# Kernel tuning notes

Hardware: AMD Instinct MI355X
Metric: run time of the kernel (lower is better)

The kernel has to match this reference:

```python
import jax, jax.numpy as jnp
import numpy as np

GRID_SIZE = 5
SPLINE_ORDER = 3
NUM_BASIS = GRID_SIZE + SPLINE_ORDER  # 8
GRID = jnp.linspace(-1.0, 1.0, GRID_SIZE + 2 * SPLINE_ORDER + 1)  # [12]
EPS = 1e-6


def bspline_basis(x):
    """Iterative Cox-de Boor. x: [...]; returns [..., NUM_BASIS]."""
    xe = x[..., None]
    # order-0 indicator basis: [..., G-1]
    B = ((xe >= GRID[:-1]) & (xe < GRID[1:])).astype(x.dtype)
    for k in range(1, SPLINE_ORDER + 1):
        nb = B.shape[-1] - 1
        g_i = GRID[:nb]
        g_i1 = GRID[1:1 + nb]
        g_ik = GRID[k:k + nb]
        g_ik1 = GRID[k + 1:k + 1 + nb]
        dl = g_ik - g_i
        dr = g_ik1 - g_i1
        left = jnp.where(dl > EPS, (xe - g_i) / jnp.where(dl > EPS, dl, 1.0), 0.0) * B[..., :nb]
        right = jnp.where(dr > EPS, (g_ik1 - xe) / jnp.where(dr > EPS, dr, 1.0), 0.0) * B[..., 1:nb + 1]
        B = left + right
    return B[..., :NUM_BASIS]


def setup_inputs() -> dict:
    key = jax.random.key(0)
    k1, k2 = jax.random.split(key)
    x = jax.random.normal(k1, (8192, 512), dtype=jnp.float32)
    spline_coeffs = jax.random.normal(k2, (512, 512, NUM_BASIS), dtype=jnp.float32) * 0.1
    return {"x": x, "spline_coeffs": spline_coeffs}


def reference(x, spline_coeffs):
    xn = jnp.tanh(x)                       # [B, in]
    basis = bspline_basis(xn)              # [B, in, K]
    # output[b, o] = sum_{i,k} coeffs[o, i, k] * basis[b, i, k]
    return jnp.einsum('bik,oik->bo', basis, spline_coeffs)
```

## Files before the change

kernel.cpp:

```cpp
#include <hip/hip_runtime.h>
#include <hip/hip_bf16.h>
#include <stdint.h>


#define M_TOTAL 8192
#define N_DIM   512
#define K_DIM   4096
#define BM 128
#define BN 128
#define BK 64
#define NT_HALF 32
#define GRP_LDS 65536
#define BUF_HALF 32768

typedef __attribute__((ext_vector_type(8))) short short8;
typedef __attribute__((ext_vector_type(4))) float f32x4;

typedef const __attribute__((address_space(1))) uint32_t ga_u32;
typedef __attribute__((address_space(3))) uint32_t ls_u32;

__device__ __forceinline__ void gload_lds16(const void* g, void* l) {
  __builtin_amdgcn_global_load_lds((ga_u32*)(uintptr_t)g,
                                   (ls_u32*)(uint32_t)(uintptr_t)l, 16, 0, 0);
}

__device__ __forceinline__ uint32_t f2bf(float f) {
  uint32_t u = __builtin_bit_cast(uint32_t, f);
  return (u + 0x7FFFu + ((u >> 16) & 1u)) >> 16;
}

__device__ __forceinline__ void basis_slots(float xv, uint32_t o[4]) {
  xv = fminf(15.f, fmaxf(-15.f, xv));
  float e  = __expf(2.0f * xv);
  float t  = (e - 1.0f) * __builtin_amdgcn_rcpf(e + 1.0f);
  float uf = (t + 1.0f) * 5.5f;
  int   c  = (int)uf;  c = c > 10 ? 10 : c;
  float u  = uf - (float)c;
  float u2 = u * u, u3 = u2 * u, om = 1.0f - u;
  float w0 = om * om * om * (1.0f / 6.0f);
  float w1 = (3.0f * u3 - 6.0f * u2 + 4.0f) * (1.0f / 6.0f);
  float w2 = (-3.0f * u3 + 3.0f * u2 + 3.0f * u + 1.0f) * (1.0f / 6.0f);
  float w3 = u3 * (1.0f / 6.0f);
  uint32_t p01 = f2bf(w0) | (f2bf(w1) << 16);
  uint32_t p23 = f2bf(w2) | (f2bf(w3) << 16);
  uint64_t W = (uint64_t)p01 | ((uint64_t)p23 << 32);
  int d = c - 3;
  uint64_t lo = (d < 0) ? (W >> ((-d) * 16))
              : ((d < 4) ? (W << (d * 16)) : 0ull);
  uint64_t hi = (d <= 0) ? 0ull
              : ((d < 4) ? (W >> ((4 - d) * 16)) : (W << ((d - 4) * 16)));
  o[0] = (uint32_t)lo; o[1] = (uint32_t)(lo >> 32);
  o[2] = (uint32_t)hi; o[3] = (uint32_t)(hi >> 32);
}

__global__ __launch_bounds__(256) void cvt_kernel(const float* __restrict__ c,
                                                  __hip_bfloat16* __restrict__ Bt,
                                                  int total8) {
  int idx = blockIdx.x * 256 + threadIdx.x;
  if (idx >= total8) return;
  const float4* cp = reinterpret_cast<const float4*>(c) + (size_t)idx * 2;
  float4 a = cp[0], b = cp[1];
  union { unsigned short us[8]; int4 v; } pk;
  pk.us[0] = f2bf(a.x); pk.us[1] = f2bf(a.y);
  pk.us[2] = f2bf(a.z); pk.us[3] = f2bf(a.w);
  pk.us[4] = f2bf(b.x); pk.us[5] = f2bf(b.y);
  pk.us[6] = f2bf(b.z); pk.us[7] = f2bf(b.w);
  reinterpret_cast<int4*>(Bt)[idx] = pk.v;
}

__global__ __launch_bounds__(512, 2) void fused_kernel(
    const float* __restrict__ x,
    const __hip_bfloat16* __restrict__ Bt,
    float* __restrict__ C) {
  __shared__ char lds[2 * GRP_LDS];

  const int tid   = threadIdx.x;
  const int wid   = tid >> 6;
  const int lane  = tid & 63;
  const int quad  = lane >> 4;
  const int l16   = lane & 15;
  const int kgrp  = wid >> 2;
  const int w2    = wid & 3;
  const int waveM = w2 >> 1, waveN = w2 & 1;
  const int tg    = tid & 255;

  int b = blockIdx.x;
  int mt = (b & 7) * 8 + ((b >> 3) >> 2);
  int nt = (b >> 3) & 3;
  const int m0 = mt * BM, n0 = nt * BN;

  char* grp = lds + kgrp * GRP_LDS;

  uint32_t bGlob[4], sOff[4], xBase[4], aWr[4];
#pragma unroll
  for (int t = 0; t < 4; ++t) {
    int s = t * 256 + tg, row = s >> 3, p = s & 7;
    sOff[t]  = (uint32_t)s * 16u;
    bGlob[t] = (uint32_t)(n0 + row) * K_DIM + (uint32_t)(p ^ (row & 7)) * 8u
             + (uint32_t)kgrp * 2048u;
    xBase[t] = (uint32_t)(m0 + row) * 512u + (uint32_t)kgrp * 256u + (uint32_t)p;
    aWr[t]   = (uint32_t)(row * 8 + (p ^ (row & 7))) * 16u;
  }

  uint32_t aOff[2][4], bOff[2][4];
#pragma unroll
  for (int kk = 0; kk < 2; ++kk) {
    int c = kk * 4 + quad;
#pragma unroll
    for (int mi = 0; mi < 4; ++mi) {
      int row = waveM * 64 + mi * 16 + l16;
      aOff[kk][mi] = (uint32_t)(row * 8 + (c ^ (row & 7))) * 16u;
    }
#pragma unroll
    for (int ni = 0; ni < 4; ++ni) {
      int row = waveN * 64 + ni * 16 + l16;
      bOff[kk][ni] = 16384u + (uint32_t)(row * 8 + (c ^ (row & 7))) * 16u;
    }
  }

  f32x4 acc[4][4];
#pragma unroll
  for (int mi = 0; mi < 4; ++mi)
#pragma unroll
    for (int ni = 0; ni < 4; ++ni)
      acc[mi][ni] = (f32x4){0.f, 0.f, 0.f, 0.f};

#pragma unroll
  for (int t = 0; t < 4; ++t)
    gload_lds16(Bt + bGlob[t], grp + 16384 + sOff[t]);
#pragma unroll
  for (int t = 0; t < 4; ++t) {
    uint32_t o[4]; basis_slots(x[xBase[t]], o);
    *reinterpret_cast<int4*>(grp + aWr[t]) = make_int4(o[0], o[1], o[2], o[3]);
  }

  for (int it = 0; it < NT_HALF; ++it) {
    const int cur = it & 1;
    char* bufc = grp + cur * BUF_HALF;
    __syncthreads();
    if (it + 1 < NT_HALF) {
      char* bufn = grp + (1 - cur) * BUF_HALF;
      uint32_t kOff = (uint32_t)(it + 1) * 64u;
#pragma unroll
      for (int t = 0; t < 4; ++t)
        gload_lds16(Bt + bGlob[t] + kOff, bufn + 16384 + sOff[t]);
#pragma unroll
      for (int t = 0; t < 4; ++t) {
        uint32_t o[4]; basis_slots(x[xBase[t] + (uint32_t)(it + 1) * 8u], o);
        *reinterpret_cast<int4*>(bufn + aWr[t]) = make_int4(o[0], o[1], o[2], o[3]);
      }
    }
#pragma unroll
    for (int kk = 0; kk < 2; ++kk) {
      short8 af[4], bf[4];
#pragma unroll
      for (int mi = 0; mi < 4; ++mi)
        af[mi] = *reinterpret_cast<const short8*>(bufc + aOff[kk][mi]);
#pragma unroll
      for (int ni = 0; ni < 4; ++ni)
        bf[ni] = *reinterpret_cast<const short8*>(bufc + bOff[kk][ni]);
#pragma unroll
      for (int mi = 0; mi < 4; ++mi)
#pragma unroll
        for (int ni = 0; ni < 4; ++ni)
          acc[mi][ni] = __builtin_amdgcn_mfma_f32_16x16x32_bf16(
              af[mi], bf[ni], acc[mi][ni], 0, 0, 0);
    }
  }

  __syncthreads();
  if (kgrp == 1) {
#pragma unroll
    for (int mi = 0; mi < 4; ++mi)
#pragma unroll
      for (int ni = 0; ni < 4; ++ni) {
        int f = mi * 4 + ni;
        *reinterpret_cast<f32x4*>(lds + w2 * 16384 + f * 1024 + lane * 16) =
            acc[mi][ni];
      }
  }
  __syncthreads();
  if (kgrp == 0) {
#pragma unroll
    for (int mi = 0; mi < 4; ++mi) {
#pragma unroll
      for (int ni = 0; ni < 4; ++ni) {
        int f = mi * 4 + ni;
        f32x4 other = *reinterpret_cast<f32x4*>(
            lds + w2 * 16384 + f * 1024 + lane * 16);
        f32x4 s = acc[mi][ni] + other;
        int col = n0 + waveN * 64 + ni * 16 + l16;
#pragma unroll
        for (int r = 0; r < 4; ++r) {
          int row = m0 + waveM * 64 + mi * 16 + quad * 4 + r;
          C[(size_t)row * N_DIM + col] = s[r];
        }
      }
    }
  }
}

extern "C" void kernel_launch(void* const* d_in, const int* in_sizes, int n_in,
                              void* d_out, int out_size, void* d_ws, size_t ws_size,
                              hipStream_t stream) {
  const float* x    = (const float*)d_in[0];
  const float* coef = (const float*)d_in[1];
  float* out = (float*)d_out;

  __hip_bfloat16* Bt = (__hip_bfloat16*)d_ws;

  const int total8 = N_DIM * K_DIM / 8;
  cvt_kernel<<<(total8 + 255) / 256, 256, 0, stream>>>(coef, Bt, total8);

  fused_kernel<<<(M_TOTAL / BM) * (N_DIM / BN), 512, 0, stream>>>(x, Bt, out);
}
```

Before: 147.6 us.

## Split basis computation into separate kernel and use split-K GEMM with atomics

Replaces the fused kernel, which computed B-spline bases inline while loading the weights, with a standalone basis kernel that writes a bf16 A matrix to workspace. A 256-thread GEMM kernel then streams both A and B through LDS with async global-to-LDS loads, splitting K four ways and combining partial sums with float atomic adds into a pre-zeroed output. The M dimension is processed in two halves so the A workspace can be reused. This adds extra launches, a memset, a round trip of A through memory, and atomic traffic, in exchange for more blocks and a simpler GEMM inner loop.

```diff
diff --git a/kernel.cpp b/kernel.cpp
--- a/kernel.cpp
+++ b/kernel.cpp
@@ -9,9 +9,11 @@
 #define BM 128
 #define BN 128
 #define BK 64
-#define NT_HALF 32
-#define GRP_LDS 65536
-#define BUF_HALF 32768
+#define KSPLIT 4
+#define MHALF  4096
+#define KCHUNK (K_DIM / KSPLIT)
+#define NT     (KCHUNK / BK)
+#define BUF_BYTES ((BM + BN) * BK * 2)
 
 typedef __attribute__((ext_vector_type(8))) short short8;
 typedef __attribute__((ext_vector_type(4))) float f32x4;
@@ -53,6 +55,16 @@
   o[2] = (uint32_t)hi; o[3] = (uint32_t)(hi >> 32);
 }
 
+__global__ __launch_bounds__(256) void basis_kernel(const float* __restrict__ x,
+                                                    __hip_bfloat16* __restrict__ A,
+                                                    int total) {
+  int idx = blockIdx.x * 256 + threadIdx.x;
+  if (idx >= total) return;
+  uint32_t o[4];
+  basis_slots(x[idx], o);
+  reinterpret_cast<int4*>(A)[idx] = make_int4(o[0], o[1], o[2], o[3]);
+}
+
 __global__ __launch_bounds__(256) void cvt_kernel(const float* __restrict__ c,
                                                   __hip_bfloat16* __restrict__ Bt,
                                                   int total8) {
@@ -61,45 +73,44 @@
   const float4* cp = reinterpret_cast<const float4*>(c) + (size_t)idx * 2;
   float4 a = cp[0], b = cp[1];
   union { unsigned short us[8]; int4 v; } pk;
-  pk.us[0] = f2bf(a.x); pk.us[1] = f2bf(a.y);
-  pk.us[2] = f2bf(a.z); pk.us[3] = f2bf(a.w);
-  pk.us[4] = f2bf(b.x); pk.us[5] = f2bf(b.y);
-  pk.us[6] = f2bf(b.z); pk.us[7] = f2bf(b.w);
+  pk.us[0] = (unsigned short)f2bf(a.x); pk.us[1] = (unsigned short)f2bf(a.y);
+  pk.us[2] = (unsigned short)f2bf(a.z); pk.us[3] = (unsigned short)f2bf(a.w);
+  pk.us[4] = (unsigned short)f2bf(b.x); pk.us[5] = (unsigned short)f2bf(b.y);
+  pk.us[6] = (unsigned short)f2bf(b.z); pk.us[7] = (unsigned short)f2bf(b.w);
   reinterpret_cast<int4*>(Bt)[idx] = pk.v;
 }
 
-__global__ __launch_bounds__(512, 2) void fused_kernel(
-    const float* __restrict__ x,
+__global__ __launch_bounds__(256) void gemm_kernel(
+    const __hip_bfloat16* __restrict__ A,
     const __hip_bfloat16* __restrict__ Bt,
     float* __restrict__ C) {
-  __shared__ char lds[2 * GRP_LDS];
+  __shared__ __hip_bfloat16 lds[2 * (BM + BN) * BK];
 
   const int tid   = threadIdx.x;
   const int wid   = tid >> 6;
   const int lane  = tid & 63;
   const int quad  = lane >> 4;
   const int l16   = lane & 15;
-  const int kgrp  = wid >> 2;
-  const int w2    = wid & 3;
-  const int waveM = w2 >> 1, waveN = w2 & 1;
-  const int tg    = tid & 255;
-
-  int b = blockIdx.x;
-  int mt = (b & 7) * 8 + ((b >> 3) >> 2);
-  int nt = (b >> 3) & 3;
-  const int m0 = mt * BM, n0 = nt * BN;
-
-  char* grp = lds + kgrp * GRP_LDS;
-
-  uint32_t bGlob[4], sOff[4], xBase[4], aWr[4];
+  const int waveM = wid >> 1;
+  const int waveN = wid & 1;
+
+  const int b   = blockIdx.x;
+  const int xcd = b & 7;
+  const int q   = b >> 3;
+  const int mt  = xcd * 4 + (q >> 4);
+  const int nt  = (q >> 2) & 3;
+  const int ks  = q & 3;
+  const int m0  = mt * BM;
+  const int n0  = nt * BN;
+  const uint32_t kbase = (uint32_t)ks * KCHUNK;
+
+  uint32_t aGlob[4], bGlob[4], sOff[4];
 #pragma unroll
   for (int t = 0; t < 4; ++t) {
-    int s = t * 256 + tg, row = s >> 3, p = s & 7;
+    int s = t * 256 + tid, row = s >> 3, p = s & 7, cc = p ^ (row & 7);
     sOff[t]  = (uint32_t)s * 16u;
-    bGlob[t] = (uint32_t)(n0 + row) * K_DIM + (uint32_t)(p ^ (row & 7)) * 8u
-             + (uint32_t)kgrp * 2048u;
-    xBase[t] = (uint32_t)(m0 + row) * 512u + (uint32_t)kgrp * 256u + (uint32_t)p;
-    aWr[t]   = (uint32_t)(row * 8 + (p ^ (row & 7))) * 16u;
+    aGlob[t] = (uint32_t)(m0 + row) * K_DIM + (uint32_t)cc * 8u + kbase;
+    bGlob[t] = (uint32_t)(n0 + row) * K_DIM + (uint32_t)cc * 8u + kbase;
   }
 
   uint32_t aOff[2][4], bOff[2][4];
@@ -118,6 +129,8 @@
     }
   }
 
+  char* ldsc = (char*)lds;
+
   f32x4 acc[4][4];
 #pragma unroll
   for (int mi = 0; mi < 4; ++mi)
@@ -126,28 +139,22 @@
       acc[mi][ni] = (f32x4){0.f, 0.f, 0.f, 0.f};
 
 #pragma unroll
-  for (int t = 0; t < 4; ++t)
-    gload_lds16(Bt + bGlob[t], grp + 16384 + sOff[t]);
-#pragma unroll
   for (int t = 0; t < 4; ++t) {
-    uint32_t o[4]; basis_slots(x[xBase[t]], o);
-    *reinterpret_cast<int4*>(grp + aWr[t]) = make_int4(o[0], o[1], o[2], o[3]);
-  }
-
-  for (int it = 0; it < NT_HALF; ++it) {
+    gload_lds16(A + aGlob[t], ldsc + sOff[t]);
+    gload_lds16(Bt + bGlob[t], ldsc + 16384 + sOff[t]);
+  }
+
+  for (int it = 0; it < NT; ++it) {
     const int cur = it & 1;
-    char* bufc = grp + cur * BUF_HALF;
+    char* bufc = ldsc + cur * BUF_BYTES;
     __syncthreads();
-    if (it + 1 < NT_HALF) {
-      char* bufn = grp + (1 - cur) * BUF_HALF;
-      uint32_t kOff = (uint32_t)(it + 1) * 64u;
-#pragma unroll
-      for (int t = 0; t < 4; ++t)
-        gload_lds16(Bt + bGlob[t] + kOff, bufn + 16384 + sOff[t]);
+    if (it + 1 < NT) {
+      char* bufn = ldsc + (1 - cur) * BUF_BYTES;
+      uint32_t kt = (uint32_t)(it + 1) * BK;
 #pragma unroll
       for (int t = 0; t < 4; ++t) {
-        uint32_t o[4]; basis_slots(x[xBase[t] + (uint32_t)(it + 1) * 8u], o);
-        *reinterpret_cast<int4*>(bufn + aWr[t]) = make_int4(o[0], o[1], o[2], o[3]);
+        gload_lds16(A + aGlob[t] + kt, bufn + sOff[t]);
+        gload_lds16(Bt + bGlob[t] + kt, bufn + 16384 + sOff[t]);
       }
     }
 #pragma unroll
@@ -168,33 +175,15 @@
     }
   }
 
-  __syncthreads();
-  if (kgrp == 1) {
-#pragma unroll
-    for (int mi = 0; mi < 4; ++mi)
-#pragma unroll
-      for (int ni = 0; ni < 4; ++ni) {
-        int f = mi * 4 + ni;
-        *reinterpret_cast<f32x4*>(lds + w2 * 16384 + f * 1024 + lane * 16) =
-            acc[mi][ni];
-      }
-  }
-  __syncthreads();
-  if (kgrp == 0) {
-#pragma unroll
-    for (int mi = 0; mi < 4; ++mi) {
-#pragma unroll
-      for (int ni = 0; ni < 4; ++ni) {
-        int f = mi * 4 + ni;
-        f32x4 other = *reinterpret_cast<f32x4*>(
-            lds + w2 * 16384 + f * 1024 + lane * 16);
-        f32x4 s = acc[mi][ni] + other;
-        int col = n0 + waveN * 64 + ni * 16 + l16;
-#pragma unroll
-        for (int r = 0; r < 4; ++r) {
-          int row = m0 + waveM * 64 + mi * 16 + quad * 4 + r;
-          C[(size_t)row * N_DIM + col] = s[r];
-        }
+#pragma unroll
+  for (int mi = 0; mi < 4; ++mi) {
+#pragma unroll
+    for (int ni = 0; ni < 4; ++ni) {
+      int col = n0 + waveN * 64 + ni * 16 + l16;
+#pragma unroll
+      for (int r = 0; r < 4; ++r) {
+        int row = m0 + waveM * 64 + mi * 16 + quad * 4 + r;
+        unsafeAtomicAdd(&C[(size_t)row * N_DIM + col], acc[mi][ni][r]);
       }
     }
   }
@@ -208,9 +197,18 @@
   float* out = (float*)d_out;
 
   __hip_bfloat16* Bt = (__hip_bfloat16*)d_ws;
+  __hip_bfloat16* A  = (__hip_bfloat16*)((char*)d_ws + (size_t)4 * 1024 * 1024);
+
+  hipMemsetAsync(d_out, 0, (size_t)out_size * sizeof(float), stream);
 
   const int total8 = N_DIM * K_DIM / 8;
   cvt_kernel<<<(total8 + 255) / 256, 256, 0, stream>>>(coef, Bt, total8);
 
-  fused_kernel<<<(M_TOTAL / BM) * (N_DIM / BN), 512, 0, stream>>>(x, Bt, out);
-}
+  for (int half = 0; half < 2; ++half) {
+    const int total = MHALF * 512;
+    basis_kernel<<<total / 256, 256, 0, stream>>>(
+        x + (size_t)half * MHALF * 512, A, total);
+    gemm_kernel<<<(MHALF / BM) * (N_DIM / BN) * KSPLIT, 256, 0, stream>>>(
+        A, Bt, out + (size_t)half * MHALF * N_DIM);
+  }
+}
```

New measurement: 172.8 us. 17.0% more time.

## Unfuse B-spline basis computation into a separate kernel feeding a pure GEMM

Applied to the files above, without the earlier changes.

Moves the tanh and B-spline basis evaluation out of the GEMM mainloop into a standalone kernel that writes a bf16 A matrix (8192x4096) to workspace. The GEMM then loads both A and B tiles with async global-to-LDS loads instead of computing basis values in registers and storing them to LDS. This removes per-tile ALU work and the four-way recomputation of the basis across N tiles, at the cost of an extra kernel launch and writing then reading a 64 MB intermediate. The launch bounds also drop the min-2-blocks hint.

```diff
diff --git a/kernel.cpp b/kernel.cpp
--- a/kernel.cpp
+++ b/kernel.cpp
@@ -53,6 +53,16 @@
   o[2] = (uint32_t)hi; o[3] = (uint32_t)(hi >> 32);
 }
 
+__global__ __launch_bounds__(256) void basis_kernel(const float* __restrict__ x,
+                                                    __hip_bfloat16* __restrict__ A,
+                                                    int total) {
+  int idx = blockIdx.x * 256 + threadIdx.x;
+  if (idx >= total) return;
+  uint32_t o[4];
+  basis_slots(x[idx], o);
+  reinterpret_cast<int4*>(A)[idx] = make_int4(o[0], o[1], o[2], o[3]);
+}
+
 __global__ __launch_bounds__(256) void cvt_kernel(const float* __restrict__ c,
                                                   __hip_bfloat16* __restrict__ Bt,
                                                   int total8) {
@@ -61,15 +71,15 @@
   const float4* cp = reinterpret_cast<const float4*>(c) + (size_t)idx * 2;
   float4 a = cp[0], b = cp[1];
   union { unsigned short us[8]; int4 v; } pk;
-  pk.us[0] = f2bf(a.x); pk.us[1] = f2bf(a.y);
-  pk.us[2] = f2bf(a.z); pk.us[3] = f2bf(a.w);
-  pk.us[4] = f2bf(b.x); pk.us[5] = f2bf(b.y);
-  pk.us[6] = f2bf(b.z); pk.us[7] = f2bf(b.w);
+  pk.us[0] = (unsigned short)f2bf(a.x); pk.us[1] = (unsigned short)f2bf(a.y);
+  pk.us[2] = (unsigned short)f2bf(a.z); pk.us[3] = (unsigned short)f2bf(a.w);
+  pk.us[4] = (unsigned short)f2bf(b.x); pk.us[5] = (unsigned short)f2bf(b.y);
+  pk.us[6] = (unsigned short)f2bf(b.z); pk.us[7] = (unsigned short)f2bf(b.w);
   reinterpret_cast<int4*>(Bt)[idx] = pk.v;
 }
 
-__global__ __launch_bounds__(512, 2) void fused_kernel(
-    const float* __restrict__ x,
+__global__ __launch_bounds__(512) void gemm_kernel(
+    const __hip_bfloat16* __restrict__ A,
     const __hip_bfloat16* __restrict__ Bt,
     float* __restrict__ C) {
   __shared__ char lds[2 * GRP_LDS];
@@ -84,22 +94,24 @@
   const int waveM = w2 >> 1, waveN = w2 & 1;
   const int tg    = tid & 255;
 
-  int b = blockIdx.x;
-  int mt = (b & 7) * 8 + ((b >> 3) >> 2);
-  int nt = (b >> 3) & 3;
-  const int m0 = mt * BM, n0 = nt * BN;
+  const int b  = blockIdx.x;
+  const int q  = b >> 3;
+  const int mt = (b & 7) * 8 + (q >> 2);
+  const int nt = q & 3;
+  const int m0 = mt * BM;
+  const int n0 = nt * BN;
 
   char* grp = lds + kgrp * GRP_LDS;
 
-  uint32_t bGlob[4], sOff[4], xBase[4], aWr[4];
+  uint32_t aGlob[4], bGlob[4], sOff[4];
 #pragma unroll
   for (int t = 0; t < 4; ++t) {
-    int s = t * 256 + tg, row = s >> 3, p = s & 7;
+    int s = t * 256 + tg, row = s >> 3, p = s & 7, cc = p ^ (row & 7);
     sOff[t]  = (uint32_t)s * 16u;
-    bGlob[t] = (uint32_t)(n0 + row) * K_DIM + (uint32_t)(p ^ (row & 7)) * 8u
+    aGlob[t] = (uint32_t)(m0 + row) * K_DIM + (uint32_t)cc * 8u
              + (uint32_t)kgrp * 2048u;
-    xBase[t] = (uint32_t)(m0 + row) * 512u + (uint32_t)kgrp * 256u + (uint32_t)p;
-    aWr[t]   = (uint32_t)(row * 8 + (p ^ (row & 7))) * 16u;
+    bGlob[t] = (uint32_t)(n0 + row) * K_DIM + (uint32_t)cc * 8u
+             + (uint32_t)kgrp * 2048u;
   }
 
   uint32_t aOff[2][4], bOff[2][4];
@@ -126,12 +138,9 @@
       acc[mi][ni] = (f32x4){0.f, 0.f, 0.f, 0.f};
 
 #pragma unroll
-  for (int t = 0; t < 4; ++t)
+  for (int t = 0; t < 4; ++t) {
+    gload_lds16(A + aGlob[t], grp + sOff[t]);
     gload_lds16(Bt + bGlob[t], grp + 16384 + sOff[t]);
-#pragma unroll
-  for (int t = 0; t < 4; ++t) {
-    uint32_t o[4]; basis_slots(x[xBase[t]], o);
-    *reinterpret_cast<int4*>(grp + aWr[t]) = make_int4(o[0], o[1], o[2], o[3]);
   }
 
   for (int it = 0; it < NT_HALF; ++it) {
@@ -140,14 +149,11 @@
     __syncthreads();
     if (it + 1 < NT_HALF) {
       char* bufn = grp + (1 - cur) * BUF_HALF;
-      uint32_t kOff = (uint32_t)(it + 1) * 64u;
-#pragma unroll
-      for (int t = 0; t < 4; ++t)
-        gload_lds16(Bt + bGlob[t] + kOff, bufn + 16384 + sOff[t]);
+      uint32_t kt = (uint32_t)(it + 1) * BK;
 #pragma unroll
       for (int t = 0; t < 4; ++t) {
-        uint32_t o[4]; basis_slots(x[xBase[t] + (uint32_t)(it + 1) * 8u], o);
-        *reinterpret_cast<int4*>(bufn + aWr[t]) = make_int4(o[0], o[1], o[2], o[3]);
+        gload_lds16(A + aGlob[t] + kt, bufn + sOff[t]);
+        gload_lds16(Bt + bGlob[t] + kt, bufn + 16384 + sOff[t]);
       }
     }
 #pragma unroll
@@ -208,9 +214,13 @@
   float* out = (float*)d_out;
 
   __hip_bfloat16* Bt = (__hip_bfloat16*)d_ws;
+  __hip_bfloat16* A  = (__hip_bfloat16*)((char*)d_ws + (size_t)4 * 1024 * 1024);
 
   const int total8 = N_DIM * K_DIM / 8;
   cvt_kernel<<<(total8 + 255) / 256, 256, 0, stream>>>(coef, Bt, total8);
 
-  fused_kernel<<<(M_TOTAL / BM) * (N_DIM / BN), 512, 0, stream>>>(x, Bt, out);
-}
+  const int total = M_TOTAL * 512;
+  basis_kernel<<<total / 256, 256, 0, stream>>>(x, A, total);
+
+  gemm_kernel<<<(M_TOTAL / BM) * (N_DIM / BN), 512, 0, stream>>>(A, Bt, out);
+}
```

Result: faster. 119.8 us (-18.8%).
